# Kernel optimization log

Measured on AMD Instinct MI355X. Metric: run time of the kernel, lower is better.

Reference implementation:

```python
import jax, jax.numpy as jnp
import numpy as np
from jax import lax

H, HH = 512, 256          # hidden_size, per-direction TLSTM hidden
B, S = 16, 4096
NOTE_V, CHUNK_V = 512, 512
NUM_LABELS = 1
STD = 0.02                # initializer_range
LN_EPS = 1e-12


def setup_inputs() -> dict:
    key = jax.random.key(0)
    ks = jax.random.split(key, 12)
    n = lambda k, s: jax.random.normal(k, s, jnp.float32) * STD
    return {
        "inputs": jax.random.normal(ks[0], (B, S, H), jnp.float32),
        "times": jax.random.uniform(ks[1], (B, S, 1), jnp.float32),
        "new_note_ids": jax.random.randint(ks[2], (B, S), 0, NOTE_V),
        "new_chunk_ids": jax.random.randint(ks[3], (B, S), 0, CHUNK_V),
        "note_emb": n(ks[4], (NOTE_V, H)),
        "chunk_emb": n(ks[5], (CHUNK_V, H)),
        "W_comb": n(ks[6], (3 * H, H)),
        "b_comb": jnp.zeros((H,), jnp.float32),
        "ln_g": jnp.ones((H,), jnp.float32),
        "ln_b": jnp.zeros((H,), jnp.float32),
        "Wx": n(ks[7], (2, 4, H, HH)),    # [dir, gate(i,f,o,c), in, hid]
        "Wh": n(ks[8], (2, 4, HH, HH)),
        "bg": jnp.zeros((2, 4, HH), jnp.float32),
        "Wd": n(ks[9], (2, HH, HH)),      # W_decomp per direction
        "bd": jnp.zeros((2, HH), jnp.float32),
        "W_cls": n(ks[10], (H, NUM_LABELS)),
        "b_cls": jnp.zeros((NUM_LABELS,), jnp.float32),
    }


def _run_dir(xseq, tseq, Wx, Wh, bg, Wd, bd):
    # xseq: [S,B,H], tseq: [S,B,1]
    def step(carry, xt):
        h, c = carry
        x, t = xt
        T = 1.0 / jnp.log(t + jnp.e)                  # time decay, [B,1] -> broadcast [B,HH]
        c_st = jnp.tanh(c @ Wd + bd)                  # short-term memory
        c_adj = c - c_st + T * c_st                   # discounted cell
        g = jax.nn.sigmoid(jnp.einsum('bd,kdh->kbh', x, Wx)
                           + jnp.einsum('bh,kho->kbo', h, Wh)
                           + bg[:, None, :])          # note: candidate uses sigmoid in original
        i, f, o, cg = g[0], g[1], g[2], g[3]
        ct = f * c_adj + i * cg
        hn = o * jnp.tanh(ct)
        return (hn, ct), hn
    z = jnp.zeros((xseq.shape[1], Wh.shape[-1]), xseq.dtype)
    _, hs = lax.scan(step, (z, z), (xseq, tseq))
    return hs  # [S,B,HH]


def reference(inputs, times, new_note_ids, new_chunk_ids, note_emb, chunk_emb,
              W_comb, b_comb, ln_g, ln_b, Wx, Wh, bg, Wd, bd, W_cls, b_cls):
    # PatientLevelEmbedding (embed_mode='all'), dropout = identity (eval)
    x = jnp.concatenate([inputs, note_emb[new_note_ids], chunk_emb[new_chunk_ids]],
                        axis=-1) @ W_comb + b_comb
    mu = jnp.mean(x, -1, keepdims=True)
    var = jnp.mean((x - mu) ** 2, -1, keepdims=True)
    x = (x - mu) / jnp.sqrt(var + LN_EPS) * ln_g + ln_b

    xs = jnp.transpose(x, (1, 0, 2))      # [S,B,H]  (batch_first permute)
    ts = jnp.transpose(times, (1, 0, 2))  # [S,B,1]

    hs_f = _run_dir(xs, ts, Wx[0], Wh[0], bg[0], Wd[0], bd[0])
    # backward pass: time at step 0 is times[0], then flipped times shifted by one
    t_bwd = jnp.concatenate([ts[:1], jnp.flip(ts, 0)[:-1]], axis=0)
    hs_b = _run_dir(jnp.flip(xs, 0), t_bwd, Wx[1], Wh[1], bg[1], Wd[1], bd[1])

    hidden = jnp.concatenate([hs_f, hs_b], axis=-1)   # [S,B,2*HH]
    drop_in = hidden[-1, 0, :]                        # == lstm_output[0, -1, :] batch-first
    logits = drop_in @ W_cls + b_cls
    logits = jnp.where(jnp.isnan(logits) | jnp.isinf(logits), 0.0, logits)
    pred = jax.nn.sigmoid(logits)
    pred = jnp.where(jnp.isnan(pred) | jnp.isinf(pred), 0.0, pred)
    return pred
```

## Files before the change

kernel.cpp:

```cpp
#include <hip/hip_runtime.h>
#include <math.h>

#define SQ 4096
#define HD 512
#define HHD 256
#define TS 8

#define BAR_LDS() asm volatile("s_waitcnt lgkmcnt(0)\n\ts_barrier" ::: "memory")
#define FENCE_LDS() asm volatile("s_waitcnt lgkmcnt(0)" ::: "memory")
#define COMPILER_BARRIER() asm volatile("" ::: "memory")

typedef _Float16 h2 __attribute__((ext_vector_type(2)));

__device__ __forceinline__ h2 u2h(unsigned v) { union { unsigned u; h2 h; } x; x.u = v; return x.h; }
__device__ __forceinline__ unsigned h2u(h2 v) { union { unsigned u; h2 h; } x; x.h = v; return x.u; }

__device__ __forceinline__ float fdot2f(h2 a, h2 b, float c) {
#if __has_builtin(__builtin_amdgcn_fdot2)
  return __builtin_amdgcn_fdot2(a, b, c, false);
#else
  return fmaf((float)a.x, (float)b.x, fmaf((float)a.y, (float)b.y, c));
#endif
}

__global__ __launch_bounds__(512) void kA(const float* __restrict__ inputs,
                                          const int* __restrict__ nid,
                                          const int* __restrict__ cid,
                                          const float* __restrict__ note_emb,
                                          const float* __restrict__ chunk_emb,
                                          const float* __restrict__ Wc,
                                          const float* __restrict__ bc,
                                          float* __restrict__ xln) {
  __shared__ float xcat[TS][1536];
  const int t = threadIdx.x;
  const int s0 = blockIdx.x * TS;
  for (int si = 0; si < TS; ++si) {
    const int s = s0 + si;
    xcat[si][t]        = inputs[s * HD + t];
    xcat[si][512 + t]  = note_emb[nid[s] * HD + t];
    xcat[si][1024 + t] = chunk_emb[cid[s] * HD + t];
  }
  __syncthreads();
  float acc[TS];
  const float bcv = bc[t];
#pragma unroll
  for (int si = 0; si < TS; ++si) acc[si] = bcv;
  for (int r = 0; r < 1536; r += 4) {
    const float w0 = Wc[(r + 0) * HD + t];
    const float w1 = Wc[(r + 1) * HD + t];
    const float w2 = Wc[(r + 2) * HD + t];
    const float w3 = Wc[(r + 3) * HD + t];
#pragma unroll
    for (int si = 0; si < TS; ++si) {
      const float4 xv = *reinterpret_cast<const float4*>(&xcat[si][r]);
      acc[si] = fmaf(xv.x, w0, acc[si]);
      acc[si] = fmaf(xv.y, w1, acc[si]);
      acc[si] = fmaf(xv.z, w2, acc[si]);
      acc[si] = fmaf(xv.w, w3, acc[si]);
    }
  }
  for (int si = 0; si < TS; ++si) xln[(s0 + si) * HD + t] = acc[si];
}

__global__ __launch_bounds__(256) void kB(float* __restrict__ xln,
                                          const float* __restrict__ g,
                                          const float* __restrict__ b) {
  __shared__ float red[4];
  __shared__ float mu_s, rs_s;
  const int s = blockIdx.x;
  const int t = threadIdx.x;
  const int wave = t >> 6, lane = t & 63;
  float v0 = xln[s * HD + t];
  float v1 = xln[s * HD + t + 256];
  float sum = v0 + v1;
#pragma unroll
  for (int o = 32; o >= 1; o >>= 1) sum += __shfl_down(sum, o, 64);
  if (lane == 0) red[wave] = sum;
  __syncthreads();
  if (t == 0) mu_s = (red[0] + red[1] + red[2] + red[3]) * (1.0f / 512.0f);
  __syncthreads();
  const float mu = mu_s;
  const float d0 = v0 - mu, d1 = v1 - mu;
  float vs = d0 * d0 + d1 * d1;
#pragma unroll
  for (int o = 32; o >= 1; o >>= 1) vs += __shfl_down(vs, o, 64);
  if (lane == 0) red[wave] = vs;
  __syncthreads();
  if (t == 0) rs_s = rsqrtf((red[0] + red[1] + red[2] + red[3]) * (1.0f / 512.0f) + 1e-12f);
  __syncthreads();
  const float rs = rs_s;
  xln[s * HD + t]       = d0 * rs * g[t] + b[t];
  xln[s * HD + t + 256] = d1 * rs * g[t + 256] + b[t + 256];
}

__global__ __launch_bounds__(512) void kC(const float* __restrict__ xln,
                                          const float* __restrict__ Wx,
                                          const float* __restrict__ bg,
                                          float* __restrict__ gx) {
  __shared__ float xs[TS][HD];
  const int t = threadIdx.x;
  const int dir = blockIdx.y;
  const int s0 = blockIdx.x * TS;
  for (int si = 0; si < TS; ++si) {
    const int sx = dir ? (SQ - 1 - (s0 + si)) : (s0 + si);
    xs[si][t] = xln[sx * HD + t];
  }
  __syncthreads();
  const int k1 = t >> 8, j = t & 255;
  const int k2 = k1 + 2;
  const float* w1 = Wx + (size_t)(dir * 4 + k1) * HD * HHD + j;
  const float* w2 = Wx + (size_t)(dir * 4 + k2) * HD * HHD + j;
  float acc1[TS], acc2[TS];
  const float b1 = bg[(dir * 4 + k1) * HHD + j];
  const float b2 = bg[(dir * 4 + k2) * HHD + j];
#pragma unroll
  for (int si = 0; si < TS; ++si) { acc1[si] = b1; acc2[si] = b2; }
  for (int d = 0; d < HD; d += 4) {
    const float w1a = w1[(d + 0) * HHD], w1b = w1[(d + 1) * HHD];
    const float w1c = w1[(d + 2) * HHD], w1d = w1[(d + 3) * HHD];
    const float w2a = w2[(d + 0) * HHD], w2b = w2[(d + 1) * HHD];
    const float w2c = w2[(d + 2) * HHD], w2d = w2[(d + 3) * HHD];
#pragma unroll
    for (int si = 0; si < TS; ++si) {
      const float4 xv = *reinterpret_cast<const float4*>(&xs[si][d]);
      acc1[si] = fmaf(xv.x, w1a, acc1[si]);
      acc1[si] = fmaf(xv.y, w1b, acc1[si]);
      acc1[si] = fmaf(xv.z, w1c, acc1[si]);
      acc1[si] = fmaf(xv.w, w1d, acc1[si]);
      acc2[si] = fmaf(xv.x, w2a, acc2[si]);
      acc2[si] = fmaf(xv.y, w2b, acc2[si]);
      acc2[si] = fmaf(xv.z, w2c, acc2[si]);
      acc2[si] = fmaf(xv.w, w2d, acc2[si]);
    }
  }
  for (int si = 0; si < TS; ++si) {
    float* row = gx + ((size_t)(dir * SQ + s0 + si)) * 1024;
    row[t]       = acc1[si];
    row[t + 512] = acc2[si];
  }
}

__device__ __forceinline__ float tanh_fast(float x) {
  const float ax = fabsf(x);
  const float e  = __expf(-2.0f * ax);
  const float t  = __fdividef(1.0f - e, 1.0f + e);
  return copysignf(t, x);
}

#define DOTQ(hu_, cu_, i_) { \
  const h2 hp_ = u2h(hu_); \
  a0 = fdot2f(wh[(i_)],      hp_, a0); \
  a1 = fdot2f(wh[32 + (i_)], hp_, a1); \
  a2 = fdot2f(wh[64 + (i_)], hp_, a2); \
  a3 = fdot2f(wh[96 + (i_)], hp_, a3); \
  ad = fdot2f(wd[(i_)], u2h(cu_), ad); }

__global__ __launch_bounds__(512, 2) void kR(const float* __restrict__ gx,
                                             const float* __restrict__ Wh,
                                             const float* __restrict__ Wd,
                                             const float* __restrict__ bd,
                                             const float* __restrict__ times,
                                             unsigned long long* __restrict__ comm,
                                             float* __restrict__ hfin) {
  const int slot = blockIdx.x & 7;
  if (slot >= 2) return;
  const int dir = slot;
  const int wg  = blockIdx.x >> 3;
  const int t   = threadIdx.x;
  const int tt  = t & 127;
  const int sk  = t >> 7;
  const int skl = sk & 1;
  const bool own = (sk < 2);
  const int j   = wg * 128 + tt;
  const int lane = t & 63;

  unsigned long long* mybase = comm + (size_t)((dir * 2 + wg) * 2) * 128;
  const unsigned long long* pbase = comm + (size_t)((dir * 2 + (wg ^ 1)) * 2) * 128;

  const int basep = (wg ^ (sk >> 1)) * 64 + skl * 32;

  h2 wh[128];
#pragma unroll
  for (int i = 0; i < 128; ++i) {
    const int k = i >> 5, p = i & 31;
    const int row = 2 * (basep + p);
    const float w0 = Wh[((size_t)(dir * 4 + k) * HHD + row) * HHD + j];
    const float w1 = Wh[((size_t)(dir * 4 + k) * HHD + row + 1) * HHD + j];
    h2 v; v.x = (_Float16)w0; v.y = (_Float16)w1;
    wh[i] = v;
  }
  h2 wd[32];
#pragma unroll
  for (int i = 0; i < 32; ++i) {
    const int row = 2 * (basep + i);
    const float w0 = Wd[(size_t)dir * HHD * HHD + (size_t)row * HHD + j];
    const float w1 = Wd[(size_t)dir * HHD * HHD + (size_t)(row + 1) * HHD + j];
    h2 v; v.x = (_Float16)w0; v.y = (_Float16)w1;
    wd[i] = v;
  }

  __shared__ __align__(16) unsigned own_h[64];
  __shared__ __align__(16) unsigned own_c[64];
  __shared__ __align__(16) unsigned pscr[2][64];
  __shared__ float pg[2][4][4][128];
  __shared__ float pd[2][4][128];
  __shared__ unsigned hflag[2];
  __shared__ float T_pre[SQ];

  for (int s = t; s < SQ; s += 512) {
    const int sidx = dir ? ((s == 0) ? 0 : (SQ - s)) : s;
    T_pre[s] = 1.0f / logf(times[sidx] + 2.7182818284590452354f);
  }
  if (t < 64) { own_h[t] = 0u; own_c[t] = 0u; }
  if (t == 0) { hflag[0] = 0u; hflag[1] = 0u; }
  __syncthreads();

  const float bdv = (t < 128) ? bd[dir * HHD + j] : 0.0f;
  const float* gxd = gx + (size_t)dir * SQ * 1024 + j;
  float g0 = 0, g1 = 0, g2 = 0, g3 = 0;
  if (t < 128) { g0 = gxd[0]; g1 = gxd[256]; g2 = gxd[512]; g3 = gxd[768]; }

  float h_my = 0.0f, c_my = 0.0f;

  const int pslot = (lane < 32) ? (skl * 32 + lane) : (64 + skl * 32 + (lane - 32));
  volatile unsigned* hf = hflag;

  for (int s = 0; s < SQ; ++s) {
    const int par = s & 1;
    float n0 = 0, n1 = 0, n2 = 0, n3 = 0;
    if (t < 128 && s + 1 < SQ) {
      const float* row = gxd + (size_t)(s + 1) * 1024;
      n0 = row[0]; n1 = row[256]; n2 = row[512]; n3 = row[768];
    }

    const uint4* hp4;
    const uint4* cp4;
    if (own) {
      while (hf[0] != (unsigned)s || hf[1] != (unsigned)s) {}
      COMPILER_BARRIER();
      hp4 = (const uint4*)&own_h[skl * 32];
      cp4 = (const uint4*)&own_c[skl * 32];
    } else {
      unsigned pv = 0u;
      if (s > 0) {
        const unsigned long long* cptr = pbase + (size_t)((s + 1) & 1) * 128 + pslot;
        unsigned long long v;
        do {
          v = __hip_atomic_load(cptr, __ATOMIC_RELAXED, __HIP_MEMORY_SCOPE_AGENT);
        } while (__any((int)((unsigned)(v >> 32) != (unsigned)s)));
        pv = (unsigned)v;
      }
      pscr[skl][lane] = pv;
      FENCE_LDS();
      hp4 = (const uint4*)&pscr[skl][0];
      cp4 = (const uint4*)&pscr[skl][32];
    }

    float a0 = 0, a1 = 0, a2 = 0, a3 = 0, ad = 0;
#pragma unroll
    for (int c4 = 0; c4 < 8; ++c4) {
      const uint4 H = hp4[c4];
      const uint4 C = cp4[c4];
      DOTQ(H.x, C.x, 4 * c4 + 0)
      DOTQ(H.y, C.y, 4 * c4 + 1)
      DOTQ(H.z, C.z, 4 * c4 + 2)
      DOTQ(H.w, C.w, 4 * c4 + 3)
    }
    pg[par][0][sk][tt] = a0;
    pg[par][1][sk][tt] = a1;
    pg[par][2][sk][tt] = a2;
    pg[par][3][sk][tt] = a3;
    pd[par][sk][tt]    = ad;
    BAR_LDS();

    if (t < 128) {
      const float s0 = pg[par][0][0][tt] + pg[par][0][1][tt] + pg[par][0][2][tt] + pg[par][0][3][tt];
      const float s1 = pg[par][1][0][tt] + pg[par][1][1][tt] + pg[par][1][2][tt] + pg[par][1][3][tt];
      const float s2 = pg[par][2][0][tt] + pg[par][2][1][tt] + pg[par][2][2][tt] + pg[par][2][3][tt];
      const float s3 = pg[par][3][0][tt] + pg[par][3][1][tt] + pg[par][3][2][tt] + pg[par][3][3][tt];
      const float sd = pd[par][0][tt] + pd[par][1][tt] + pd[par][2][tt] + pd[par][3][tt];
      const float iv  = __fdividef(1.0f, 1.0f + __expf(-(s0 + g0)));
      const float fv  = __fdividef(1.0f, 1.0f + __expf(-(s1 + g1)));
      const float ov  = __fdividef(1.0f, 1.0f + __expf(-(s2 + g2)));
      const float cgv = __fdividef(1.0f, 1.0f + __expf(-(s3 + g3)));
      const float c_st = tanh_fast(sd + bdv);
      const float T = T_pre[s];
      const float c_adj = c_my + (T - 1.0f) * c_st;
      const float ct = fv * c_adj + iv * cgv;
      const float hn = ov * tanh_fast(ct);
      c_my = ct;
      h_my = hn;
      const float hn_o = __shfl(hn, lane ^ 1, 64);
      const float ct_o = __shfl(ct, lane ^ 1, 64);
      if ((lane & 1) == 0) {
        h2 hp_; hp_.x = (_Float16)hn; hp_.y = (_Float16)hn_o;
        h2 cp_; cp_.x = (_Float16)ct; cp_.y = (_Float16)ct_o;
        const unsigned hu = h2u(hp_), cu = h2u(cp_);
        const int pl = tt >> 1;
        unsigned long long* chunk = (unsigned long long*)mybase + (size_t)par * 128;
        const unsigned long long tg = ((unsigned long long)(unsigned)(s + 1)) << 32;
        __hip_atomic_store(chunk + pl,      tg | hu, __ATOMIC_RELAXED, __HIP_MEMORY_SCOPE_AGENT);
        __hip_atomic_store(chunk + 64 + pl, tg | cu, __ATOMIC_RELAXED, __HIP_MEMORY_SCOPE_AGENT);
        own_h[pl] = hu;
        own_c[pl] = cu;
      }
      FENCE_LDS();
      if (t == 0)  hf[0] = (unsigned)(s + 1);
      if (t == 64) hf[1] = (unsigned)(s + 1);
      g0 = n0; g1 = n1; g2 = n2; g3 = n3;
    }
  }
  if (t < 128) hfin[dir * HHD + j] = h_my;
}

__global__ __launch_bounds__(512) void kD(const float* __restrict__ hfin,
                                          const float* __restrict__ Wcls,
                                          const float* __restrict__ bcls,
                                          float* __restrict__ out) {
  __shared__ float red[8];
  const int t = threadIdx.x;
  float v = hfin[t] * Wcls[t];
#pragma unroll
  for (int o = 32; o >= 1; o >>= 1) v += __shfl_down(v, o, 64);
  if ((t & 63) == 0) red[t >> 6] = v;
  __syncthreads();
  if (t == 0) {
    float l = red[0] + red[1] + red[2] + red[3] + red[4] + red[5] + red[6] + red[7] + bcls[0];
    if (isnan(l) || isinf(l)) l = 0.0f;
    float p = 1.0f / (1.0f + expf(-l));
    if (isnan(p) || isinf(p)) p = 0.0f;
    out[0] = p;
  }
}

extern "C" void kernel_launch(void* const* d_in, const int* in_sizes, int n_in,
                              void* d_out, int out_size, void* d_ws, size_t ws_size,
                              hipStream_t stream) {
  const float* inputs    = (const float*)d_in[0];
  const float* times     = (const float*)d_in[1];
  const int*   nid       = (const int*)d_in[2];
  const int*   cid       = (const int*)d_in[3];
  const float* note_emb  = (const float*)d_in[4];
  const float* chunk_emb = (const float*)d_in[5];
  const float* W_comb    = (const float*)d_in[6];
  const float* b_comb    = (const float*)d_in[7];
  const float* ln_g      = (const float*)d_in[8];
  const float* ln_b      = (const float*)d_in[9];
  const float* Wx        = (const float*)d_in[10];
  const float* Wh        = (const float*)d_in[11];
  const float* bg        = (const float*)d_in[12];
  const float* Wd        = (const float*)d_in[13];
  const float* bd        = (const float*)d_in[14];
  const float* W_cls     = (const float*)d_in[15];
  const float* b_cls     = (const float*)d_in[16];

  float* ws   = (float*)d_ws;
  float* xln  = ws;
  float* gx   = ws + (size_t)SQ * HD;
  float* hfin = gx + (size_t)2 * SQ * 1024;
  unsigned long long* comm = (unsigned long long*)(hfin + 512);

  kA<<<SQ / TS, 512, 0, stream>>>(inputs, nid, cid, note_emb, chunk_emb, W_comb, b_comb, xln);
  kB<<<SQ, 256, 0, stream>>>(xln, ln_g, ln_b);
  kC<<<dim3(SQ / TS, 2), 512, 0, stream>>>(xln, Wx, bg, gx);
  kR<<<10, 512, 0, stream>>>(gx, Wh, Wd, bd, times, comm, hfin);
  kD<<<1, 512, 0, stream>>>(hfin, W_cls, b_cls, (float*)d_out);
}
```

Baseline: 7.291 ms.

## Split recurrent kernel across four workgroups per direction instead of two

The recurrent kernel now spreads each direction's 256 hidden units over four workgroups of 64 units instead of two of 128. Each workgroup keeps a smaller register-resident slice of the fp16 weights and exchanges h/c with three peer workgroups through tagged global atomics. This shortens the per-step dot-product work and register pressure (launch bounds raised to four blocks). The cost is more cross-workgroup synchronization per step and a longer LDS reduction over 8 slices. Spin loops gain an iteration guard, and the local spin now sleeps between polls.

```diff
diff --git a/kernel.cpp b/kernel.cpp
--- a/kernel.cpp
+++ b/kernel.cpp
@@ -150,12 +150,14 @@
 #define DOTQ(hu_, cu_, i_) { \
   const h2 hp_ = u2h(hu_); \
   a0 = fdot2f(wh[(i_)],      hp_, a0); \
-  a1 = fdot2f(wh[32 + (i_)], hp_, a1); \
-  a2 = fdot2f(wh[64 + (i_)], hp_, a2); \
-  a3 = fdot2f(wh[96 + (i_)], hp_, a3); \
+  a1 = fdot2f(wh[16 + (i_)], hp_, a1); \
+  a2 = fdot2f(wh[32 + (i_)], hp_, a2); \
+  a3 = fdot2f(wh[48 + (i_)], hp_, a3); \
   ad = fdot2f(wd[(i_)], u2h(cu_), ad); }
 
-__global__ __launch_bounds__(512, 2) void kR(const float* __restrict__ gx,
+#define SPIN_GUARD (1u << 20)
+
+__global__ __launch_bounds__(512, 4) void kR(const float* __restrict__ gx,
                                              const float* __restrict__ Wh,
                                              const float* __restrict__ Wd,
                                              const float* __restrict__ bd,
@@ -165,33 +167,33 @@
   const int slot = blockIdx.x & 7;
   if (slot >= 2) return;
   const int dir = slot;
-  const int wg  = blockIdx.x >> 3;
+  const int w   = blockIdx.x >> 3;
   const int t   = threadIdx.x;
-  const int tt  = t & 127;
-  const int sk  = t >> 7;
-  const int skl = sk & 1;
-  const bool own = (sk < 2);
-  const int j   = wg * 128 + tt;
-  const int lane = t & 63;
-
-  unsigned long long* mybase = comm + (size_t)((dir * 2 + wg) * 2) * 128;
-  const unsigned long long* pbase = comm + (size_t)((dir * 2 + (wg ^ 1)) * 2) * 128;
-
-  const int basep = (wg ^ (sk >> 1)) * 64 + skl * 32;
-
-  h2 wh[128];
-#pragma unroll
-  for (int i = 0; i < 128; ++i) {
-    const int k = i >> 5, p = i & 31;
+  const int tt  = t & 63;
+  const int sk  = t >> 6;
+  const int hh  = sk & 1;
+  const int owner = (w + (sk >> 1)) & 3;
+  const bool own  = (sk < 2);
+  const int j   = w * 64 + tt;
+
+  unsigned long long* mybase = comm + (size_t)((dir * 4 + w) * 2) * 64;
+  const unsigned long long* obase = comm + (size_t)((dir * 4 + owner) * 2) * 64;
+
+  const int basep = owner * 32 + hh * 16;
+
+  h2 wh[64];
+#pragma unroll
+  for (int i = 0; i < 64; ++i) {
+    const int k = i >> 4, p = i & 15;
     const int row = 2 * (basep + p);
     const float w0 = Wh[((size_t)(dir * 4 + k) * HHD + row) * HHD + j];
     const float w1 = Wh[((size_t)(dir * 4 + k) * HHD + row + 1) * HHD + j];
     h2 v; v.x = (_Float16)w0; v.y = (_Float16)w1;
     wh[i] = v;
   }
-  h2 wd[32];
-#pragma unroll
-  for (int i = 0; i < 32; ++i) {
+  h2 wd[16];
+#pragma unroll
+  for (int i = 0; i < 16; ++i) {
     const int row = 2 * (basep + i);
     const float w0 = Wd[(size_t)dir * HHD * HHD + (size_t)row * HHD + j];
     const float w1 = Wd[(size_t)dir * HHD * HHD + (size_t)(row + 1) * HHD + j];
@@ -199,36 +201,37 @@
     wd[i] = v;
   }
 
-  __shared__ __align__(16) unsigned own_h[64];
-  __shared__ __align__(16) unsigned own_c[64];
-  __shared__ __align__(16) unsigned pscr[2][64];
-  __shared__ float pg[2][4][4][128];
-  __shared__ float pd[2][4][128];
-  __shared__ unsigned hflag[2];
+  __shared__ __align__(16) unsigned own_h[32];
+  __shared__ __align__(16) unsigned own_c[32];
+  __shared__ __align__(16) unsigned pscr[6][32];
+  __shared__ float pg[2][4][8][64];
+  __shared__ float pd[2][8][64];
+  __shared__ unsigned hflag[1];
   __shared__ float T_pre[SQ];
 
   for (int s = t; s < SQ; s += 512) {
     const int sidx = dir ? ((s == 0) ? 0 : (SQ - s)) : s;
     T_pre[s] = 1.0f / logf(times[sidx] + 2.7182818284590452354f);
   }
-  if (t < 64) { own_h[t] = 0u; own_c[t] = 0u; }
-  if (t == 0) { hflag[0] = 0u; hflag[1] = 0u; }
-  __syncthreads();
-
-  const float bdv = (t < 128) ? bd[dir * HHD + j] : 0.0f;
+  if (t < 32) { own_h[t] = 0u; own_c[t] = 0u; }
+  if (t == 0) hflag[0] = 0u;
+  __syncthreads();
+
+  const float bdv = (t < 64) ? bd[dir * HHD + j] : 0.0f;
   const float* gxd = gx + (size_t)dir * SQ * 1024 + j;
   float g0 = 0, g1 = 0, g2 = 0, g3 = 0;
-  if (t < 128) { g0 = gxd[0]; g1 = gxd[256]; g2 = gxd[512]; g3 = gxd[768]; }
+  if (t < 64) { g0 = gxd[0]; g1 = gxd[256]; g2 = gxd[512]; g3 = gxd[768]; }
 
   float h_my = 0.0f, c_my = 0.0f;
 
-  const int pslot = (lane < 32) ? (skl * 32 + lane) : (64 + skl * 32 + (lane - 32));
+  const int l31 = tt & 31;
+  const int pslot = (l31 < 16) ? (hh * 16 + l31) : (32 + hh * 16 + (l31 - 16));
   volatile unsigned* hf = hflag;
 
   for (int s = 0; s < SQ; ++s) {
     const int par = s & 1;
     float n0 = 0, n1 = 0, n2 = 0, n3 = 0;
-    if (t < 128 && s + 1 < SQ) {
+    if (t < 64 && s + 1 < SQ) {
       const float* row = gxd + (size_t)(s + 1) * 1024;
       n0 = row[0]; n1 = row[256]; n2 = row[512]; n3 = row[768];
     }
@@ -236,29 +239,32 @@
     const uint4* hp4;
     const uint4* cp4;
     if (own) {
-      while (hf[0] != (unsigned)s || hf[1] != (unsigned)s) {}
+      unsigned gd = 0;
+      while (hf[0] != (unsigned)s && ++gd < SPIN_GUARD) __builtin_amdgcn_s_sleep(1);
       COMPILER_BARRIER();
-      hp4 = (const uint4*)&own_h[skl * 32];
-      cp4 = (const uint4*)&own_c[skl * 32];
+      hp4 = (const uint4*)&own_h[hh * 16];
+      cp4 = (const uint4*)&own_c[hh * 16];
     } else {
       unsigned pv = 0u;
       if (s > 0) {
-        const unsigned long long* cptr = pbase + (size_t)((s + 1) & 1) * 128 + pslot;
+        const unsigned long long* cptr = obase + (size_t)((s + 1) & 1) * 64 + pslot;
+        const unsigned tag = (unsigned)s;
         unsigned long long v;
+        unsigned gd = 0;
         do {
           v = __hip_atomic_load(cptr, __ATOMIC_RELAXED, __HIP_MEMORY_SCOPE_AGENT);
-        } while (__any((int)((unsigned)(v >> 32) != (unsigned)s)));
+        } while (__any((int)((unsigned)(v >> 32) != tag)) && ++gd < SPIN_GUARD);
         pv = (unsigned)v;
       }
-      pscr[skl][lane] = pv;
+      pscr[sk - 2][l31] = pv;
       FENCE_LDS();
-      hp4 = (const uint4*)&pscr[skl][0];
-      cp4 = (const uint4*)&pscr[skl][32];
+      hp4 = (const uint4*)&pscr[sk - 2][0];
+      cp4 = (const uint4*)&pscr[sk - 2][16];
     }
 
     float a0 = 0, a1 = 0, a2 = 0, a3 = 0, ad = 0;
 #pragma unroll
-    for (int c4 = 0; c4 < 8; ++c4) {
+    for (int c4 = 0; c4 < 4; ++c4) {
       const uint4 H = hp4[c4];
       const uint4 C = cp4[c4];
       DOTQ(H.x, C.x, 4 * c4 + 0)
@@ -273,12 +279,16 @@
     pd[par][sk][tt]    = ad;
     BAR_LDS();
 
-    if (t < 128) {
-      const float s0 = pg[par][0][0][tt] + pg[par][0][1][tt] + pg[par][0][2][tt] + pg[par][0][3][tt];
-      const float s1 = pg[par][1][0][tt] + pg[par][1][1][tt] + pg[par][1][2][tt] + pg[par][1][3][tt];
-      const float s2 = pg[par][2][0][tt] + pg[par][2][1][tt] + pg[par][2][2][tt] + pg[par][2][3][tt];
-      const float s3 = pg[par][3][0][tt] + pg[par][3][1][tt] + pg[par][3][2][tt] + pg[par][3][3][tt];
-      const float sd = pd[par][0][tt] + pd[par][1][tt] + pd[par][2][tt] + pd[par][3][tt];
+    if (t < 64) {
+      float s0 = 0, s1 = 0, s2 = 0, s3 = 0, sd = 0;
+#pragma unroll
+      for (int sl = 0; sl < 8; ++sl) {
+        s0 += pg[par][0][sl][tt];
+        s1 += pg[par][1][sl][tt];
+        s2 += pg[par][2][sl][tt];
+        s3 += pg[par][3][sl][tt];
+        sd += pd[par][sl][tt];
+      }
       const float iv  = __fdividef(1.0f, 1.0f + __expf(-(s0 + g0)));
       const float fv  = __fdividef(1.0f, 1.0f + __expf(-(s1 + g1)));
       const float ov  = __fdividef(1.0f, 1.0f + __expf(-(s2 + g2)));
@@ -290,27 +300,26 @@
       const float hn = ov * tanh_fast(ct);
       c_my = ct;
       h_my = hn;
-      const float hn_o = __shfl(hn, lane ^ 1, 64);
-      const float ct_o = __shfl(ct, lane ^ 1, 64);
-      if ((lane & 1) == 0) {
+      const float hn_o = __shfl(hn, tt ^ 1, 64);
+      const float ct_o = __shfl(ct, tt ^ 1, 64);
+      if ((tt & 1) == 0) {
         h2 hp_; hp_.x = (_Float16)hn; hp_.y = (_Float16)hn_o;
         h2 cp_; cp_.x = (_Float16)ct; cp_.y = (_Float16)ct_o;
         const unsigned hu = h2u(hp_), cu = h2u(cp_);
         const int pl = tt >> 1;
-        unsigned long long* chunk = (unsigned long long*)mybase + (size_t)par * 128;
+        unsigned long long* chunk = (unsigned long long*)mybase + (size_t)par * 64;
         const unsigned long long tg = ((unsigned long long)(unsigned)(s + 1)) << 32;
         __hip_atomic_store(chunk + pl,      tg | hu, __ATOMIC_RELAXED, __HIP_MEMORY_SCOPE_AGENT);
-        __hip_atomic_store(chunk + 64 + pl, tg | cu, __ATOMIC_RELAXED, __HIP_MEMORY_SCOPE_AGENT);
+        __hip_atomic_store(chunk + 32 + pl, tg | cu, __ATOMIC_RELAXED, __HIP_MEMORY_SCOPE_AGENT);
         own_h[pl] = hu;
         own_c[pl] = cu;
       }
       FENCE_LDS();
-      if (t == 0)  hf[0] = (unsigned)(s + 1);
-      if (t == 64) hf[1] = (unsigned)(s + 1);
+      if (t == 0) hf[0] = (unsigned)(s + 1);
       g0 = n0; g1 = n1; g2 = n2; g3 = n3;
     }
   }
-  if (t < 128) hfin[dir * HHD + j] = h_my;
+  if (t < 64) hfin[dir * HHD + j] = h_my;
 }
 
 __global__ __launch_bounds__(512) void kD(const float* __restrict__ hfin,
@@ -363,6 +372,6 @@
   kA<<<SQ / TS, 512, 0, stream>>>(inputs, nid, cid, note_emb, chunk_emb, W_comb, b_comb, xln);
   kB<<<SQ, 256, 0, stream>>>(xln, ln_g, ln_b);
   kC<<<dim3(SQ / TS, 2), 512, 0, stream>>>(xln, Wx, bg, gx);
-  kR<<<10, 512, 0, stream>>>(gx, Wh, Wd, bd, times, comm, hfin);
+  kR<<<26, 512, 0, stream>>>(gx, Wh, Wd, bd, times, comm, hfin);
   kD<<<1, 512, 0, stream>>>(hfin, W_cls, b_cls, (float*)d_out);
 }
```

Result: slower. 8.514 ms (+16.8%).
